# Kernel optimization log

Measured on AMD Instinct MI355X. Metric: run time of the kernel, lower is better.

Reference implementation:

```python
import jax, jax.numpy as jnp
import numpy as np

B, N, M, C = 4, 4096, 300, 1152
SA_H, SA_D = 36, 32           # linear self-attention heads / head dim
CA_H = 16                     # cross-attention heads
INNER_SA = SA_H * SA_D        # 1152
INNER_FF = int(C * 2.5)       # 2880
EPS = 1e-6


def _ln(x):
    # LayerNorm without affine, eps=1e-6
    mu = x.mean(-1, keepdims=True)
    var = x.var(-1, keepdims=True)
    return (x - mu) / jnp.sqrt(var + EPS)


def setup_inputs() -> dict:
    key = jax.random.key(0)
    ks = jax.random.split(key, 24)
    p = lambda i, shape: jax.random.normal(ks[i], shape, jnp.float32) * 0.02
    return {
        "x": jax.random.normal(ks[0], (B, N, C), jnp.float32),
        "conditioning": jax.random.normal(ks[1], (B, M, C), jnp.float32),
        "t_emb": jax.random.normal(ks[2], (B, C), jnp.float32),
        # linear self-attention (qkv has no bias)
        "w_qkv": p(3, (C, 3 * INNER_SA)),
        "w_sa_out": p(4, (INNER_SA, C)),
        "b_sa_out": jnp.zeros((C,), jnp.float32),
        # norm_cross (affine LayerNorm)
        "gamma_cross": jnp.ones((C,), jnp.float32),
        "beta_cross": jnp.zeros((C,), jnp.float32),
        # cross-attention
        "w_q": p(5, (C, C)), "b_q": jnp.zeros((C,), jnp.float32),
        "w_kv": p(6, (C, 2 * C)), "b_kv": jnp.zeros((2 * C,), jnp.float32),
        "w_co": p(7, (C, C)), "b_co": jnp.zeros((C,), jnp.float32),
        # MixFFN
        "w_fc1": p(8, (C, 2 * INNER_FF)), "b_fc1": jnp.zeros((2 * INNER_FF,), jnp.float32),
        "dw_kernel": p(9, (3, 3, 1, INNER_FF)),  # depthwise conv, HWIO
        "dw_bias": jnp.zeros((INNER_FF,), jnp.float32),
        "w_fc2": p(10, (INNER_FF, C)), "b_fc2": jnp.zeros((C,), jnp.float32),
        # adaLN modulation
        "w_ada": p(11, (C, 6 * C)), "b_ada": jnp.zeros((6 * C,), jnp.float32),
        "sst": jax.random.normal(ks[12], (6, C), jnp.float32) * 0.02,
    }


def reference(x, conditioning, t_emb, w_qkv, w_sa_out, b_sa_out,
              gamma_cross, beta_cross, w_q, b_q, w_kv, b_kv, w_co, b_co,
              w_fc1, b_fc1, dw_kernel, dw_bias, w_fc2, b_fc2,
              w_ada, b_ada, sst):
    Bx, Nx, Cx = x.shape
    ada = jax.nn.silu(t_emb) @ w_ada + b_ada          # (B, 6C)
    ada = sst[None] + ada.reshape(Bx, 6, Cx)          # (B, 6, C)
    shift_sa, scale_sa, gate_sa, shift_ff, scale_ff, gate_ff = (
        ada[:, 0], ada[:, 1], ada[:, 2], ada[:, 3], ada[:, 4], ada[:, 5])

    # --- modulated linear self-attention (ReLU kernel) ---
    xn = _ln(x) * (1.0 + scale_sa[:, None]) + shift_sa[:, None]
    qkv = (xn @ w_qkv).reshape(Bx, Nx, 3, SA_H, SA_D)
    q = jax.nn.relu(qkv[:, :, 0])
    k = jax.nn.relu(qkv[:, :, 1])
    v = qkv[:, :, 2]
    kv = jnp.einsum('bnhd,bnhe->bhde', k, v)                  # (B,H,D,D)
    out = jnp.einsum('bnhd,bhde->bnhe', q, kv)                # (B,N,H,D)
    denom = jnp.einsum('bnhd,bhd->bnh', q, k.sum(1)) + 1e-6   # (B,N,H)
    out = (out / denom[..., None]).reshape(Bx, Nx, INNER_SA)
    x = x + gate_sa[:, None] * (out @ w_sa_out + b_sa_out)

    # --- cross-attention (softmax) ---
    xc = _ln(x) * gamma_cross + beta_cross
    hd = Cx // CA_H
    qc = (xc @ w_q + b_q).reshape(Bx, Nx, CA_H, hd)
    kvc = (conditioning @ w_kv + b_kv).reshape(Bx, M, 2, CA_H, hd)
    kc, vc = kvc[:, :, 0], kvc[:, :, 1]
    attn = jnp.einsum('bnhd,bmhd->bhnm', qc, kc) * (hd ** -0.5)
    attn = jax.nn.softmax(attn, axis=-1)
    oc = jnp.einsum('bhnm,bmhd->bnhd', attn, vc).reshape(Bx, Nx, Cx)
    x = x + oc @ w_co + b_co

    # --- modulated GLU-dwconv FFN ---
    xn = _ln(x) * (1.0 + scale_ff[:, None]) + shift_ff[:, None]
    gv = xn @ w_fc1 + b_fc1
    gate, val = gv[..., :INNER_FF], gv[..., INNER_FF:]
    h = jax.nn.silu(gate) * val
    hw = int(round(Nx ** 0.5))
    h = h.reshape(Bx, hw, hw, INNER_FF)                       # NHWC
    h = jax.lax.conv_general_dilated(
        h, dw_kernel, window_strides=(1, 1), padding='SAME',
        dimension_numbers=('NHWC', 'HWIO', 'NHWC'),
        feature_group_count=INNER_FF) + dw_bias
    h = h.reshape(Bx, Nx, INNER_FF)
    x = x + gate_ff[:, None] * (h @ w_fc2 + b_fc2)
    return x
```

## Files before the change

kernel.cpp:

```cpp
#include <hip/hip_runtime.h>

typedef __bf16 bf16_t;
typedef __attribute__((ext_vector_type(8))) __bf16 bf16x8;
typedef __attribute__((ext_vector_type(4))) __bf16 bf16x4;
typedef __attribute__((ext_vector_type(4))) float f32x4;

#define DEVINL __device__ __forceinline__

DEVINL void gload16(const void* g, void* l) {
  __builtin_amdgcn_global_load_lds(
      (const __attribute__((address_space(1))) void*)g,
      (__attribute__((address_space(3))) void*)l, 16, 0, 0);
}

template <int OUT>
__global__ __launch_bounds__(512) void gemm256(
    const bf16_t* __restrict__ A, const bf16_t* __restrict__ Bt,
    void* __restrict__ Cv, int M, int N, int K,
    const float* __restrict__ bias, const float* __restrict__ resid,
    const float* __restrict__ gate, int GM)
{
  __shared__ __align__(16) bf16_t sA[2][256 * 64];
  __shared__ __align__(16) bf16_t sB[2][256 * 64];
  const int tid = threadIdx.x;
  const int lane = tid & 63;
  const int wave = tid >> 6;
  const int wr = wave >> 2;
  const int wc = wave & 3;

  const int nbx = gridDim.x, nby = gridDim.y;
  const int nwg = nbx * nby;
  int lin = (int)blockIdx.y * nbx + (int)blockIdx.x;
  {
    const int q = nwg >> 3, r = nwg & 7;
    const int xcd = lin & 7, idx = lin >> 3;
    lin = (xcd < r ? xcd * (q + 1) : r * (q + 1) + (xcd - r) * q) + idx;
  }
  const int per_grp = GM * nbx;
  const int gid = lin / per_grp;
  const int rem = lin - gid * per_grp;
  const int gsz = min(GM, nby - gid * GM);
  const long tileM = (long)(gid * GM + rem % gsz) * 256;
  const long tileN = (long)(rem / gsz) * 256;

  int arow[4], acol[4];
#pragma unroll
  for (int j = 0; j < 4; ++j) {
    const int ch = tid + j * 512;
    const int r = ch >> 3;
    arow[j] = r;
    acol[j] = ((ch & 7) ^ (r & 7)) * 8;
  }

  auto STAGE = [&](int buf, int kt) {
#pragma unroll
    for (int j = 0; j < 4; ++j)
      gload16(A + (tileM + arow[j]) * (long)K + kt + acol[j],
              (char*)(&sA[buf][0]) + (tid + j * 512) * 16);
#pragma unroll
    for (int j = 0; j < 4; ++j)
      gload16(Bt + (tileN + arow[j]) * (long)K + kt + acol[j],
              (char*)(&sB[buf][0]) + (tid + j * 512) * 16);
  };

  f32x4 acc[8][4] = {};
  const int NT = K >> 6;

  STAGE(0, 0);
  STAGE(1, 64);
  asm volatile("s_waitcnt vmcnt(8)" ::: "memory");
  asm volatile("s_barrier" ::: "memory");

  const int lrow = lane & 15;
  const int lkbase = (lane >> 4) << 4;
  const int lxor = (lane & 7) << 4;

  for (int t = 0; t < NT; ++t) {
    const char* pA = (const char*)(&sA[t & 1][0]);
    const char* pB = (const char*)(&sB[t & 1][0]);
#pragma unroll
    for (int ks = 0; ks < 2; ++ks) {
      const int koff = ((ks << 6) | lkbase) ^ lxor;
      bf16x8 a[8], b[4];
#pragma unroll
      for (int n = 0; n < 4; ++n)
        b[n] = *(const bf16x8*)(pB + (wc * 64 + n * 16 + lrow) * 128 + koff);
#pragma unroll
      for (int m = 0; m < 8; ++m)
        a[m] = *(const bf16x8*)(pA + (wr * 128 + m * 16 + lrow) * 128 + koff);
      __builtin_amdgcn_s_setprio(1);
#pragma unroll
      for (int m = 0; m < 8; ++m)
#pragma unroll
        for (int n = 0; n < 4; ++n)
          acc[m][n] = __builtin_amdgcn_mfma_f32_16x16x32_bf16(a[m], b[n],
                                                              acc[m][n], 0, 0, 0);
      __builtin_amdgcn_s_setprio(0);
    }
    __builtin_amdgcn_sched_barrier(0);
    asm volatile("s_barrier" ::: "memory");
    if (t + 2 < NT) {
      STAGE(t & 1, (t + 2) << 6);
      asm volatile("s_waitcnt vmcnt(8)" ::: "memory");
    } else {
      asm volatile("s_waitcnt vmcnt(0)" ::: "memory");
    }
    asm volatile("s_barrier" ::: "memory");
  }

  const long row0 = tileM + wr * 128 + ((lane >> 4) * 4);
  const int col0 = (int)tileN + wc * 64 + lrow;
#pragma unroll
  for (int m = 0; m < 8; ++m) {
#pragma unroll
    for (int n = 0; n < 4; ++n) {
      const int col = col0 + n * 16;
      if (col < N) {
        const float bb = bias ? bias[col] : 0.0f;
#pragma unroll
        for (int j = 0; j < 4; ++j) {
          const long row = row0 + m * 16 + j;
          const long idx = row * (long)N + col;
          const float v = acc[m][n][j] + bb;
          if constexpr (OUT == 1) {
            const float g = gate ? gate[(row >> 12) * 6912 + col] : 1.0f;
            const float r = resid ? resid[idx] : 0.0f;
            ((float*)Cv)[idx] = r + g * v;
          } else {
            ((bf16_t*)Cv)[idx] = (bf16_t)v;
          }
        }
      }
    }
  }
}

template <int OUT>
__global__ __launch_bounds__(256) void gemm_bt(
    const bf16_t* __restrict__ A, const bf16_t* __restrict__ Bt,
    void* __restrict__ Cv, int M, int N, int K,
    long strideA, long strideB, long strideC,
    const float* __restrict__ bias, int GM)
{
  __shared__ __align__(16) bf16_t sA[128 * 32];
  __shared__ __align__(16) bf16_t sB[128 * 32];
  const int tid = threadIdx.x;
  const int lane = tid & 63;
  const int wave = tid >> 6;
  const bf16_t* Ab = A + (size_t)blockIdx.z * strideA;
  const bf16_t* Bb = Bt + (size_t)blockIdx.z * strideB;

  const int nbx = gridDim.x, nby = gridDim.y;
  const int nwg = nbx * nby;
  int lin = (int)blockIdx.y * nbx + (int)blockIdx.x;
  {
    const int q = nwg >> 3, r = nwg & 7;
    const int xcd = lin & 7, idx = lin >> 3;
    lin = (xcd < r ? xcd * (q + 1) : r * (q + 1) + (xcd - r) * q) + idx;
  }
  const int per_grp = GM * nbx;
  const int gid = lin / per_grp;
  const int rem = lin - gid * per_grp;
  const int gsz = min(GM, nby - gid * GM);
  const long tileM = (long)(gid * GM + rem % gsz) * 128;
  const long tileN = (long)(rem / gsz) * 128;
  const int wr = wave >> 1, wc = wave & 1;

  f32x4 acc[4][4] = {};

  const int srow = lane >> 2;
  const int skcol = (lane & 3) * 8;
  const bf16_t* gA0 = Ab + (tileM + wave * 16 + srow) * (long)K + skcol;
  const bf16_t* gB0 = Bb + (tileN + wave * 16 + srow) * (long)K + skcol;
  bf16_t* lA0 = sA + wave * 512;
  bf16_t* lB0 = sB + wave * 512;
  const long rs64 = 64L * K;

  const int aoff = (wr * 64 + (lane & 15)) * 32 + (lane >> 4) * 8;
  const int boff = (wc * 64 + (lane & 15)) * 32 + (lane >> 4) * 8;

  for (int kt = 0; kt < K; kt += 32) {
    __syncthreads();
    gload16(gA0 + kt, lA0);
    gload16(gA0 + kt + rs64, lA0 + 2048);
    gload16(gB0 + kt, lB0);
    gload16(gB0 + kt + rs64, lB0 + 2048);
    __syncthreads();
    bf16x8 av[4], bv[4];
#pragma unroll
    for (int m = 0; m < 4; ++m) av[m] = *(const bf16x8*)&sA[aoff + m * 512];
#pragma unroll
    for (int n = 0; n < 4; ++n) bv[n] = *(const bf16x8*)&sB[boff + n * 512];
#pragma unroll
    for (int m = 0; m < 4; ++m)
#pragma unroll
      for (int n = 0; n < 4; ++n)
        acc[m][n] = __builtin_amdgcn_mfma_f32_16x16x32_bf16(av[m], bv[n],
                                                            acc[m][n], 0, 0, 0);
  }

  const long row0 = tileM + wr * 64 + ((lane >> 4) * 4);
  const int col0 = (int)tileN + wc * 64 + (lane & 15);
#pragma unroll
  for (int m = 0; m < 4; ++m) {
#pragma unroll
    for (int n = 0; n < 4; ++n) {
      const int col = col0 + n * 16;
      const float bb = (OUT != 2 && bias) ? bias[col] : 0.0f;
#pragma unroll
      for (int j = 0; j < 4; ++j) {
        const long row = row0 + m * 16 + j;
        const float v = acc[m][n][j] + bb;
        if constexpr (OUT == 2) {
          if (col < 72)
            ((bf16_t*)Cv)[row * 1152 + (long)blockIdx.z * 72 + col] = (bf16_t)v;
        } else {
          const long idx = row * (long)N + col;
          (((bf16_t*)Cv) + (size_t)blockIdx.z * strideC)[idx] = (bf16_t)v;
        }
      }
    }
  }
}

__global__ __launch_bounds__(256) void transpose_cast(
    const float* __restrict__ W, bf16_t* __restrict__ WT, int K, int N)
{
  __shared__ float tile[32][33];
  const int n0 = blockIdx.x * 32, k0 = blockIdx.y * 32;
  const int tx = threadIdx.x & 31, ty = threadIdx.x >> 5;
#pragma unroll
  for (int r = ty; r < 32; r += 8) tile[r][tx] = W[(size_t)(k0 + r) * N + n0 + tx];
  __syncthreads();
#pragma unroll
  for (int r = ty; r < 32; r += 8)
    WT[(size_t)(n0 + r) * K + k0 + tx] = (bf16_t)tile[tx][r];
}

__global__ __launch_bounds__(256) void ada_kernel(
    const float* __restrict__ t_emb, const float* __restrict__ w_ada,
    const float* __restrict__ b_ada, const float* __restrict__ sst,
    float* __restrict__ ada)
{
  __shared__ float st[4][1152];
  const int t = threadIdx.x;
  const int j = blockIdx.x * 256 + t;
  for (int i = t; i < 4 * 1152; i += 256) {
    const int b = i / 1152, cc = i % 1152;
    const float v = t_emb[b * 1152 + cc];
    st[b][cc] = v / (1.0f + __expf(-v));
  }
  __syncthreads();
  const int k0 = blockIdx.y * 144;
  float a0 = 0.f, a1 = 0.f, a2 = 0.f, a3 = 0.f;
  for (int k = k0; k < k0 + 144; ++k) {
    const float w = w_ada[(size_t)k * 6912 + j];
    a0 += st[0][k] * w; a1 += st[1][k] * w;
    a2 += st[2][k] * w; a3 += st[3][k] * w;
  }
  if (blockIdx.y == 0) {
    const float base = b_ada[j] + sst[j];
    a0 += base; a1 += base; a2 += base; a3 += base;
  }
  atomicAdd(&ada[0 * 6912 + j], a0);
  atomicAdd(&ada[1 * 6912 + j], a1);
  atomicAdd(&ada[2 * 6912 + j], a2);
  atomicAdd(&ada[3 * 6912 + j], a3);
}

__global__ __launch_bounds__(256) void ln_mod(
    const float* __restrict__ X, bf16_t* __restrict__ out,
    const float* __restrict__ adaB, int shiftIdx, int scaleIdx,
    const float* __restrict__ gamma, const float* __restrict__ beta)
{
  const int row = blockIdx.x;
  const float4* xr4 = (const float4*)(X + (size_t)row * 1152);
  float s = 0.f, s2 = 0.f;
  for (int i = threadIdx.x; i < 288; i += 256) {
    const float4 v = xr4[i];
    s += v.x + v.y + v.z + v.w;
    s2 += v.x * v.x + v.y * v.y + v.z * v.z + v.w * v.w;
  }
  const int lane = threadIdx.x & 63, wave = threadIdx.x >> 6;
#pragma unroll
  for (int o = 32; o; o >>= 1) { s += __shfl_down(s, o); s2 += __shfl_down(s2, o); }
  __shared__ float rs[4], rq[4];
  if (lane == 0) { rs[wave] = s; rq[wave] = s2; }
  __syncthreads();
  if (threadIdx.x == 0) {
    rs[0] = rs[0] + rs[1] + rs[2] + rs[3];
    rq[0] = rq[0] + rq[1] + rq[2] + rq[3];
  }
  __syncthreads();
  const float mu = rs[0] * (1.0f / 1152.0f);
  const float var = rq[0] * (1.0f / 1152.0f) - mu * mu;
  const float inv = rsqrtf(var + 1e-6f);
  const int b = row >> 12;
  const float4* shiftv = (const float4*)(adaB ? adaB + b * 6912 + shiftIdx * 1152 : beta);
  const float4* scalev = (const float4*)(adaB ? adaB + b * 6912 + scaleIdx * 1152 : gamma);
  const float add1 = adaB ? 1.0f : 0.0f;
  for (int i = threadIdx.x; i < 288; i += 256) {
    const float4 v = xr4[i];
    const float4 sc = scalev[i];
    const float4 sh = shiftv[i];
    bf16x4 o;
    o[0] = (bf16_t)((v.x - mu) * inv * (add1 + sc.x) + sh.x);
    o[1] = (bf16_t)((v.y - mu) * inv * (add1 + sc.y) + sh.y);
    o[2] = (bf16_t)((v.z - mu) * inv * (add1 + sc.z) + sh.z);
    o[3] = (bf16_t)((v.w - mu) * inv * (add1 + sc.w) + sh.w);
    *(bf16x4*)&out[(size_t)row * 1152 + i * 4] = o;
  }
}

__global__ void pad_cond_k(const float* __restrict__ cond, bf16_t* __restrict__ condp)
{
  const int idx = blockIdx.x * 256 + threadIdx.x;
  const int row = idx / 1152;
  condp[idx] = (row < 1200) ? (bf16_t)cond[idx] : (bf16_t)0.0f;
}

__global__ __launch_bounds__(256) void sa_kv_k(
    const bf16_t* __restrict__ qkv, float* __restrict__ kvb, float* __restrict__ ksumb)
{
  const int bh = blockIdx.x, b = bh / 36, h = bh % 36;
  __shared__ bf16_t sk[32][32], sv[32][32];
  const int t = threadIdx.x;
  const int nn = t >> 5, c = t & 31;
  const int srow = (t & 127) >> 2;
  const int sq4 = (t & 3) * 8;
  const int isV = t >> 7;
  float a0 = 0.f, a1 = 0.f, a2 = 0.f, a3 = 0.f, ks = 0.f;
  const size_t rowbase = (size_t)b * 4096 + (size_t)blockIdx.y * 256;
  const size_t colbase = 1152 + (size_t)isV * 1152 + h * 32 + sq4;
  for (int n0 = 0; n0 < 256; n0 += 32) {
    __syncthreads();
    const bf16x8 v8 = *(const bf16x8*)&qkv[(rowbase + n0 + srow) * 3456 + colbase];
    if (isV == 0) {
      bf16x8 r8;
#pragma unroll
      for (int j = 0; j < 8; ++j) r8[j] = (bf16_t)fmaxf((float)v8[j], 0.0f);
      *(bf16x8*)&sk[srow][sq4] = r8;
    } else {
      *(bf16x8*)&sv[srow][sq4] = v8;
    }
    __syncthreads();
#pragma unroll
    for (int q = 0; q < 32; ++q) {
      const float vv = (float)sv[q][c];
      a0 += (float)sk[q][nn] * vv;
      a1 += (float)sk[q][nn + 8] * vv;
      a2 += (float)sk[q][nn + 16] * vv;
      a3 += (float)sk[q][nn + 24] * vv;
    }
    if (t < 32) {
#pragma unroll
      for (int q = 0; q < 32; ++q) ks += (float)sk[q][t];
    }
  }
  float* kvp = kvb + (size_t)bh * 1024;
  atomicAdd(&kvp[(nn + 0) * 32 + c], a0);
  atomicAdd(&kvp[(nn + 8) * 32 + c], a1);
  atomicAdd(&kvp[(nn + 16) * 32 + c], a2);
  atomicAdd(&kvp[(nn + 24) * 32 + c], a3);
  if (t < 32) atomicAdd(&ksumb[bh * 32 + t], ks);
}

__global__ __launch_bounds__(256) void sa_out_k(
    const bf16_t* __restrict__ qkv, const float* __restrict__ kvb,
    const float* __restrict__ ksumb, bf16_t* __restrict__ so)
{
  const int row0 = blockIdx.x * 8;
  const int b = row0 >> 12;
  __shared__ float q[8][1152];
  __shared__ float denom[8][36];
  const int t = threadIdx.x;
  for (int i = t; i < 1152; i += 256) {
    const int r = i / 144, c0 = (i % 144) * 8;
    const bf16x8 v8 = *(const bf16x8*)&qkv[(size_t)(row0 + r) * 3456 + c0];
#pragma unroll
    for (int j = 0; j < 8; ++j) q[r][c0 + j] = fmaxf((float)v8[j], 0.0f);
  }
  __syncthreads();
  for (int i = t; i < 288; i += 256) {
    int r = i / 36, h = i % 36;
    const float* ksp = ksumb + (b * 36 + h) * 32;
    float dsum = 1e-6f;
#pragma unroll
    for (int d = 0; d < 32; ++d) dsum += q[r][h * 32 + d] * ksp[d];
    denom[r][h] = dsum;
  }
  __syncthreads();
  for (int j = t; j < 1152; j += 256) {
    const int h = j >> 5, e = j & 31;
    const float* kvp = kvb + ((size_t)(b * 36 + h)) * 1024 + e;
    float kreg[32];
#pragma unroll
    for (int d = 0; d < 32; ++d) kreg[d] = kvp[d * 32];
#pragma unroll
    for (int r = 0; r < 8; ++r) {
      float a = 0.f;
#pragma unroll
      for (int d = 0; d < 32; ++d) a += q[r][h * 32 + d] * kreg[d];
      so[(size_t)(row0 + r) * 1152 + j] = (bf16_t)(a / denom[r][h]);
    }
  }
}

__global__ void ca_qrepack(const bf16_t* __restrict__ qc, bf16_t* __restrict__ qcp, int b)
{
  const size_t idx = (size_t)blockIdx.x * 256 + threadIdx.x;
  const int d = (int)(idx % 96);
  const size_t r = idx / 96;
  const int n = (int)(r & 4095);
  const int h = (int)(r >> 12);
  float v = 0.f;
  if (d < 72) v = (float)qc[((size_t)(b * 4096 + n)) * 1152 + h * 72 + d] * 0.11785113019775793f;
  qcp[idx] = (bf16_t)v;
}

__global__ void ca_kcrepack(const bf16_t* __restrict__ kvc, bf16_t* __restrict__ kcp, int b)
{
  const size_t idx = (size_t)blockIdx.x * 256 + threadIdx.x;
  const int d = (int)(idx % 96);
  const size_t r = idx / 96;
  const int m = (int)(r % 384);
  const int h = (int)(r / 384);
  bf16_t v = (bf16_t)0.0f;
  if (d < 72 && m < 300) v = kvc[((size_t)(b * 300 + m)) * 2304 + h * 72 + d];
  kcp[idx] = v;
}

__global__ void ca_vtrepack(const bf16_t* __restrict__ kvc, bf16_t* __restrict__ vt, int b)
{
  const size_t idx = (size_t)blockIdx.x * 256 + threadIdx.x;
  const int m = (int)(idx % 384);
  const size_t r = idx / 384;
  const int d = (int)(r & 127);
  const int h = (int)(r >> 7);
  bf16_t v = (bf16_t)0.0f;
  if (d < 72 && m < 300) v = kvc[((size_t)(b * 300 + m)) * 2304 + 1152 + h * 72 + d];
  vt[idx] = v;
}

__global__ __launch_bounds__(256) void softmax_k(bf16_t* __restrict__ s)
{
  const int row = blockIdx.x * 4 + (threadIdx.x >> 6);
  const int lane = threadIdx.x & 63;
  bf16_t* sr = s + (size_t)row * 384;
  float v[5];
  float mx = -1e30f;
#pragma unroll
  for (int i = 0; i < 5; ++i) {
    const int m = lane + 64 * i;
    v[i] = (m < 300) ? (float)sr[m] : -1e30f;
    mx = fmaxf(mx, v[i]);
  }
#pragma unroll
  for (int o = 32; o; o >>= 1) mx = fmaxf(mx, __shfl_xor(mx, o));
  float sum = 0.f;
#pragma unroll
  for (int i = 0; i < 5; ++i) { v[i] = __expf(v[i] - mx); sum += v[i]; }
#pragma unroll
  for (int o = 32; o; o >>= 1) sum += __shfl_xor(sum, o);
  const float inv = 1.0f / sum;
#pragma unroll
  for (int i = 0; i < 5; ++i) {
    const int m = lane + 64 * i;
    if (m < 320) sr[m] = (bf16_t)(v[i] * inv);
  }
}

__global__ void glu_k(const bf16_t* __restrict__ gv, bf16_t* __restrict__ h)
{
  const size_t idx = (size_t)blockIdx.x * 256 + threadIdx.x;
  const size_t row = idx / 360;
  const int c0 = (int)(idx % 360) * 8;
  const bf16x8 g8 = *(const bf16x8*)&gv[row * 5760 + c0];
  const bf16x8 v8 = *(const bf16x8*)&gv[row * 5760 + 2880 + c0];
  bf16x8 o;
#pragma unroll
  for (int j = 0; j < 8; ++j) {
    const float g = (float)g8[j];
    const float sg = g / (1.0f + __expf(-g));
    o[j] = (bf16_t)(sg * (float)v8[j]);
  }
  *(bf16x8*)&h[row * 2880 + c0] = o;
}

__global__ __launch_bounds__(256) void dwconv_k(
    const bf16_t* __restrict__ h, const float* __restrict__ wk,
    const float* __restrict__ wb, bf16_t* __restrict__ hc)
{
  const size_t idx = (size_t)blockIdx.x * 256 + threadIdx.x;
  const int c8 = (int)(idx % 360);
  size_t p = idx / 360;
  const int x = (int)(p & 63);
  const int y = (int)(p >> 6);
  const int c0 = c8 * 8;
  float acc[8];
#pragma unroll
  for (int j = 0; j < 8; ++j) acc[j] = wb[c0 + j];
  for (int ky = -1; ky <= 1; ++ky) {
    const int yy = y + ky;
    if (yy < 0 || yy > 63) continue;
    for (int kx = -1; kx <= 1; ++kx) {
      const int xx = x + kx;
      if (xx < 0 || xx > 63) continue;
      const bf16x8 v = *(const bf16x8*)&h[((size_t)(yy * 64 + xx)) * 2880 + c0];
      const float* w = wk + ((ky + 1) * 3 + (kx + 1)) * 2880 + c0;
#pragma unroll
      for (int j = 0; j < 8; ++j) acc[j] += (float)v[j] * w[j];
    }
  }
  bf16x8 o;
#pragma unroll
  for (int j = 0; j < 8; ++j) o[j] = (bf16_t)acc[j];
  *(bf16x8*)&hc[((size_t)(y * 64 + x)) * 2880 + c0] = o;
}

extern "C" void kernel_launch(void* const* d_in, const int* in_sizes, int n_in,
                              void* d_out, int out_size, void* d_ws, size_t ws_size,
                              hipStream_t stream)
{
  const float* x          = (const float*)d_in[0];
  const float* cond       = (const float*)d_in[1];
  const float* t_emb      = (const float*)d_in[2];
  const float* w_qkv      = (const float*)d_in[3];
  const float* w_sa_out   = (const float*)d_in[4];
  const float* b_sa_out   = (const float*)d_in[5];
  const float* gamma_cr   = (const float*)d_in[6];
  const float* beta_cr    = (const float*)d_in[7];
  const float* w_q        = (const float*)d_in[8];
  const float* b_q        = (const float*)d_in[9];
  const float* w_kv       = (const float*)d_in[10];
  const float* b_kv       = (const float*)d_in[11];
  const float* w_co       = (const float*)d_in[12];
  const float* b_co       = (const float*)d_in[13];
  const float* w_fc1      = (const float*)d_in[14];
  const float* b_fc1      = (const float*)d_in[15];
  const float* dw_kernel  = (const float*)d_in[16];
  const float* dw_bias    = (const float*)d_in[17];
  const float* w_fc2      = (const float*)d_in[18];
  const float* b_fc2      = (const float*)d_in[19];
  const float* w_ada      = (const float*)d_in[20];
  const float* b_ada      = (const float*)d_in[21];
  const float* sst        = (const float*)d_in[22];
  float* out = (float*)d_out;

  char* ws = (char*)d_ws;
  size_t off = 0;
  auto alloc = [&](size_t bytes) -> char* {
    off = (off + 255) & ~(size_t)255;
    char* p = ws + off;
    off += bytes;
    return p;
  };

  bf16_t* wqkvT  = (bf16_t*)alloc((size_t)3584 * 1152 * 2);
  bf16_t* wsaT   = (bf16_t*)alloc((size_t)1280 * 1152 * 2);
  bf16_t* wqT    = (bf16_t*)alloc((size_t)1280 * 1152 * 2);
  bf16_t* wkvT   = (bf16_t*)alloc((size_t)2304 * 1152 * 2);
  bf16_t* wcoT   = (bf16_t*)alloc((size_t)1280 * 1152 * 2);
  bf16_t* wfc1T  = (bf16_t*)alloc((size_t)5888 * 1152 * 2);
  bf16_t* wfc2T  = (bf16_t*)alloc((size_t)1280 * 2880 * 2);
  float*  adaB   = (float*)alloc((size_t)4 * 6912 * 4);
  bf16_t* xn     = (bf16_t*)alloc((size_t)16384 * 1152 * 2);
  bf16_t* buf37  = (bf16_t*)alloc((size_t)16384 * 1152 * 2);
  float*  kvb    = (float*)alloc((size_t)144 * 1024 * 4);
  float*  ksumb  = (float*)alloc((size_t)144 * 32 * 4);
  bf16_t* condp  = (bf16_t*)alloc((size_t)1280 * 1152 * 2);
  bf16_t* kvcB   = (bf16_t*)alloc((size_t)1280 * 2304 * 2);
  char* arena = alloc((size_t)16384 * 3456 * 2);

  if (off > ws_size) return;

  bf16_t* qkvB = (bf16_t*)arena;
  bf16_t* qcp    = (bf16_t*)arena;
  bf16_t* kcp    = (bf16_t*)(arena + 12582912);
  bf16_t* vcT    = (bf16_t*)(arena + 12582912 + 1179648);
  bf16_t* scores = (bf16_t*)(arena + 12582912 + 1179648 + 1572864);
  bf16_t* hc2b = (bf16_t*)arena;
  bf16_t* gvB  = (bf16_t*)(arena + (size_t)8192 * 2880 * 2);
  bf16_t* hB   = buf37;

  hipMemsetAsync(adaB, 0, (size_t)4 * 6912 * 4, stream);
  hipMemsetAsync(kvb, 0, (size_t)144 * 1024 * 4, stream);
  hipMemsetAsync(ksumb, 0, (size_t)144 * 32 * 4, stream);

  transpose_cast<<<dim3(108, 36), 256, 0, stream>>>(w_qkv, wqkvT, 1152, 3456);
  transpose_cast<<<dim3(36, 36), 256, 0, stream>>>(w_sa_out, wsaT, 1152, 1152);
  transpose_cast<<<dim3(36, 36), 256, 0, stream>>>(w_q, wqT, 1152, 1152);
  transpose_cast<<<dim3(72, 36), 256, 0, stream>>>(w_kv, wkvT, 1152, 2304);
  transpose_cast<<<dim3(36, 36), 256, 0, stream>>>(w_co, wcoT, 1152, 1152);
  transpose_cast<<<dim3(180, 36), 256, 0, stream>>>(w_fc1, wfc1T, 1152, 5760);
  transpose_cast<<<dim3(36, 90), 256, 0, stream>>>(w_fc2, wfc2T, 2880, 1152);
  ada_kernel<<<dim3(27, 8), 256, 0, stream>>>(t_emb, w_ada, b_ada, sst, adaB);
  pad_cond_k<<<5760, 256, 0, stream>>>(cond, condp);

  ln_mod<<<16384, 256, 0, stream>>>(x, xn, adaB, 0, 1, nullptr, nullptr);
  gemm256<0><<<dim3(14, 64), 512, 0, stream>>>(xn, wqkvT, qkvB, 16384, 3456, 1152,
                                               nullptr, nullptr, nullptr, 8);
  sa_kv_k<<<dim3(144, 16), 256, 0, stream>>>(qkvB, kvb, ksumb);
  sa_out_k<<<2048, 256, 0, stream>>>(qkvB, kvb, ksumb, buf37);
  gemm256<1><<<dim3(5, 64), 512, 0, stream>>>(buf37, wsaT, out, 16384, 1152, 1152,
                                              b_sa_out, x, adaB + 2 * 1152, 8);

  ln_mod<<<16384, 256, 0, stream>>>(out, xn, nullptr, 0, 0, gamma_cr, beta_cr);
  gemm256<0><<<dim3(5, 64), 512, 0, stream>>>(xn, wqT, buf37, 16384, 1152, 1152,
                                              b_q, nullptr, nullptr, 8);
  gemm_bt<0><<<dim3(18, 10, 1), 256, 0, stream>>>(condp, wkvT, kvcB, 1280, 2304, 1152,
                                                  0, 0, 0, b_kv, 8);
  for (int b = 0; b < 4; ++b) {
    ca_qrepack<<<24576, 256, 0, stream>>>(buf37, qcp, b);
    ca_kcrepack<<<2304, 256, 0, stream>>>(kvcB, kcp, b);
    ca_vtrepack<<<3072, 256, 0, stream>>>(kvcB, vcT, b);
    gemm_bt<0><<<dim3(3, 32, 16), 256, 0, stream>>>(qcp, kcp, scores, 4096, 384, 96,
                                                    (long)4096 * 96, (long)384 * 96,
                                                    (long)4096 * 384, nullptr, 8);
    softmax_k<<<16384, 256, 0, stream>>>(scores);
    gemm_bt<2><<<dim3(1, 32, 16), 256, 0, stream>>>(scores, vcT,
                                                    buf37 + (size_t)b * 4096 * 1152,
                                                    4096, 128, 384,
                                                    (long)4096 * 384, (long)128 * 384,
                                                    0, nullptr, 8);
  }
  gemm256<1><<<dim3(5, 64), 512, 0, stream>>>(buf37, wcoT, out, 16384, 1152, 1152,
                                              b_co, out, nullptr, 8);

  ln_mod<<<16384, 256, 0, stream>>>(out, xn, adaB, 3, 4, nullptr, nullptr);
  for (int c = 0; c < 2; ++c) {
    for (int bb = 0; bb < 2; ++bb) {
      const int b = c * 2 + bb;
      gemm256<0><<<dim3(23, 16), 512, 0, stream>>>(xn + (size_t)b * 4096 * 1152, wfc1T,
                                                   gvB, 4096, 5760, 1152,
                                                   b_fc1, nullptr, nullptr, 8);
      glu_k<<<5760, 256, 0, stream>>>(gvB, hB);
      dwconv_k<<<5760, 256, 0, stream>>>(hB, dw_kernel, dw_bias,
                                         hc2b + (size_t)bb * 4096 * 2880);
    }
    gemm256<1><<<dim3(5, 32), 512, 0, stream>>>(hc2b, wfc2T, out + (size_t)c * 8192 * 1152,
                                                8192, 1152, 2880, b_fc2,
                                                out + (size_t)c * 8192 * 1152,
                                                adaB + (size_t)c * 2 * 6912 + 5 * 1152, 8);
  }

  (void)in_sizes; (void)n_in; (void)out_size; (void)ws_size;
}
```

Baseline: 2.065 ms.

## Triple-buffer GEMM with K=32 stages and batch cross-attention and FFN launches

The main GEMM moves from a double-buffered K=64 tile to a triple-buffered K=32 tile with a new LDS swizzle and one barrier per iteration, aiming to hide global-load latency better. When the workspace is large enough, the per-batch cross-attention loop becomes single launches over all 64 batch-heads. The FFN fc1 GEMM also runs over two batches at once. This cuts launch count and gives larger grids, at the cost of a bigger workspace and a fallback path when the workspace is small.

```diff
diff --git a/kernel.cpp b/kernel.cpp
--- a/kernel.cpp
+++ b/kernel.cpp
@@ -14,14 +14,13 @@
 }
 
 template <int OUT>
-__global__ __launch_bounds__(512) void gemm256(
+__global__ __launch_bounds__(512) void gemm256r(
     const bf16_t* __restrict__ A, const bf16_t* __restrict__ Bt,
     void* __restrict__ Cv, int M, int N, int K,
     const float* __restrict__ bias, const float* __restrict__ resid,
     const float* __restrict__ gate, int GM)
 {
-  __shared__ __align__(16) bf16_t sA[2][256 * 64];
-  __shared__ __align__(16) bf16_t sB[2][256 * 64];
+  __shared__ __align__(16) bf16_t sL[3][2][256 * 32];
   const int tid = threadIdx.x;
   const int lane = tid & 63;
   const int wave = tid >> 6;
@@ -32,9 +31,9 @@
   const int nwg = nbx * nby;
   int lin = (int)blockIdx.y * nbx + (int)blockIdx.x;
   {
-    const int q = nwg >> 3, r = nwg & 7;
+    const int q = nwg >> 3, rr = nwg & 7;
     const int xcd = lin & 7, idx = lin >> 3;
-    lin = (xcd < r ? xcd * (q + 1) : r * (q + 1) + (xcd - r) * q) + idx;
+    lin = (xcd < rr ? xcd * (q + 1) : rr * (q + 1) + (xcd - rr) * q) + idx;
   }
   const int per_grp = GM * nbx;
   const int gid = lin / per_grp;
@@ -43,73 +42,60 @@
   const long tileM = (long)(gid * GM + rem % gsz) * 256;
   const long tileN = (long)(rem / gsz) * 256;
 
-  int arow[4], acol[4];
-#pragma unroll
-  for (int j = 0; j < 4; ++j) {
-    const int ch = tid + j * 512;
-    const int r = ch >> 3;
-    arow[j] = r;
-    acol[j] = ((ch & 7) ^ (r & 7)) * 8;
-  }
-
-  auto STAGE = [&](int buf, int kt) {
-#pragma unroll
-    for (int j = 0; j < 4; ++j)
-      gload16(A + (tileM + arow[j]) * (long)K + kt + acol[j],
-              (char*)(&sA[buf][0]) + (tid + j * 512) * 16);
-#pragma unroll
-    for (int j = 0; j < 4; ++j)
-      gload16(Bt + (tileN + arow[j]) * (long)K + kt + acol[j],
-              (char*)(&sB[buf][0]) + (tid + j * 512) * 16);
+  const int r0 = tid >> 2;
+  const int c0 = (((tid & 3) - (r0 >> 2)) & 3) * 8;
+
+  auto STAGE = [&](int slot, int kt) {
+    const bf16_t* ga = A + (tileM + r0) * (long)K + kt + c0;
+    const bf16_t* gb = Bt + (tileN + r0) * (long)K + kt + c0;
+    char* la = (char*)&sL[slot][0][0] + tid * 16;
+    char* lb = (char*)&sL[slot][1][0] + tid * 16;
+    gload16(ga, la);
+    gload16(ga + 128 * (long)K, la + 8192);
+    gload16(gb, lb);
+    gload16(gb + 128 * (long)K, lb + 8192);
   };
 
   f32x4 acc[8][4] = {};
-  const int NT = K >> 6;
-
-  STAGE(0, 0);
-  STAGE(1, 64);
+  const int NT = K >> 5;
+
+  STAGE(0, 0); STAGE(1, 32); STAGE(2, 64);
   asm volatile("s_waitcnt vmcnt(8)" ::: "memory");
   asm volatile("s_barrier" ::: "memory");
 
-  const int lrow = lane & 15;
-  const int lkbase = (lane >> 4) << 4;
-  const int lxor = (lane & 7) << 4;
-
+  const int r = lane & 15;
+  const int kg = lane >> 4;
+  const int sw = ((kg + (r >> 2)) & 3) * 16;
+  const int abyte = (wr * 128 + r) * 64 + sw;
+  const int bbyte = (wc * 64 + r) * 64 + sw;
+
+  int slot = 0;
   for (int t = 0; t < NT; ++t) {
-    const char* pA = (const char*)(&sA[t & 1][0]);
-    const char* pB = (const char*)(&sB[t & 1][0]);
-#pragma unroll
-    for (int ks = 0; ks < 2; ++ks) {
-      const int koff = ((ks << 6) | lkbase) ^ lxor;
-      bf16x8 a[8], b[4];
+    const char* pA = (const char*)&sL[slot][0][0];
+    const char* pB = (const char*)&sL[slot][1][0];
+    bf16x8 a[8], b[4];
+#pragma unroll
+    for (int n = 0; n < 4; ++n) b[n] = *(const bf16x8*)(pB + bbyte + n * 1024);
+#pragma unroll
+    for (int m = 0; m < 8; ++m) a[m] = *(const bf16x8*)(pA + abyte + m * 1024);
+    __builtin_amdgcn_s_setprio(1);
+#pragma unroll
+    for (int m = 0; m < 8; ++m)
 #pragma unroll
       for (int n = 0; n < 4; ++n)
-        b[n] = *(const bf16x8*)(pB + (wc * 64 + n * 16 + lrow) * 128 + koff);
-#pragma unroll
-      for (int m = 0; m < 8; ++m)
-        a[m] = *(const bf16x8*)(pA + (wr * 128 + m * 16 + lrow) * 128 + koff);
-      __builtin_amdgcn_s_setprio(1);
-#pragma unroll
-      for (int m = 0; m < 8; ++m)
-#pragma unroll
-        for (int n = 0; n < 4; ++n)
-          acc[m][n] = __builtin_amdgcn_mfma_f32_16x16x32_bf16(a[m], b[n],
-                                                              acc[m][n], 0, 0, 0);
-      __builtin_amdgcn_s_setprio(0);
-    }
-    __builtin_amdgcn_sched_barrier(0);
+        acc[m][n] = __builtin_amdgcn_mfma_f32_16x16x32_bf16(a[m], b[n],
+                                                            acc[m][n], 0, 0, 0);
+    __builtin_amdgcn_s_setprio(0);
+    if (t + 1 >= NT) break;
+    if (t + 2 < NT) asm volatile("s_waitcnt vmcnt(4)" ::: "memory");
+    else            asm volatile("s_waitcnt vmcnt(0)" ::: "memory");
     asm volatile("s_barrier" ::: "memory");
-    if (t + 2 < NT) {
-      STAGE(t & 1, (t + 2) << 6);
-      asm volatile("s_waitcnt vmcnt(8)" ::: "memory");
-    } else {
-      asm volatile("s_waitcnt vmcnt(0)" ::: "memory");
-    }
-    asm volatile("s_barrier" ::: "memory");
+    if (t + 3 < NT) STAGE(slot, (t + 3) << 5);
+    slot = (slot == 2) ? 0 : slot + 1;
   }
 
   const long row0 = tileM + wr * 128 + ((lane >> 4) * 4);
-  const int col0 = (int)tileN + wc * 64 + lrow;
+  const int col0 = (int)tileN + wc * 64 + r;
 #pragma unroll
   for (int m = 0; m < 8; ++m) {
 #pragma unroll
@@ -124,8 +110,8 @@
           const float v = acc[m][n][j] + bb;
           if constexpr (OUT == 1) {
             const float g = gate ? gate[(row >> 12) * 6912 + col] : 1.0f;
-            const float r = resid ? resid[idx] : 0.0f;
-            ((float*)Cv)[idx] = r + g * v;
+            const float rv = resid ? resid[idx] : 0.0f;
+            ((float*)Cv)[idx] = rv + g * v;
           } else {
             ((bf16_t*)Cv)[idx] = (bf16_t)v;
           }
@@ -154,9 +140,9 @@
   const int nwg = nbx * nby;
   int lin = (int)blockIdx.y * nbx + (int)blockIdx.x;
   {
-    const int q = nwg >> 3, r = nwg & 7;
+    const int q = nwg >> 3, rr = nwg & 7;
     const int xcd = lin & 7, idx = lin >> 3;
-    lin = (xcd < r ? xcd * (q + 1) : r * (q + 1) + (xcd - r) * q) + idx;
+    lin = (xcd < rr ? xcd * (q + 1) : rr * (q + 1) + (xcd - rr) * q) + idx;
   }
   const int per_grp = GM * nbx;
   const int gid = lin / per_grp;
@@ -213,7 +199,8 @@
         const float v = acc[m][n][j] + bb;
         if constexpr (OUT == 2) {
           if (col < 72)
-            ((bf16_t*)Cv)[row * 1152 + (long)blockIdx.z * 72 + col] = (bf16_t)v;
+            ((bf16_t*)Cv)[(((long)(blockIdx.z >> 4)) * 4096 + row) * 1152 +
+                          (long)(blockIdx.z & 15) * 72 + col] = (bf16_t)v;
         } else {
           const long idx = row * (long)N + col;
           (((bf16_t*)Cv) + (size_t)blockIdx.z * strideC)[idx] = (bf16_t)v;
@@ -570,18 +557,40 @@
   float*  ksumb  = (float*)alloc((size_t)144 * 32 * 4);
   bf16_t* condp  = (bf16_t*)alloc((size_t)1280 * 1152 * 2);
   bf16_t* kvcB   = (bf16_t*)alloc((size_t)1280 * 2304 * 2);
-  char* arena = alloc((size_t)16384 * 3456 * 2);
-
+
+  const size_t ARENA_SMALL = (size_t)16384 * 3456 * 2;
+  const size_t CA_Q = (size_t)64 * 4096 * 96 * 2;
+  const size_t CA_K = (size_t)64 * 384 * 96 * 2;
+  const size_t CA_V = (size_t)64 * 128 * 384 * 2;
+  const size_t CA_S = (size_t)64 * 4096 * 384 * 2;
+  const size_t ARENA_BIG = CA_Q + CA_K + CA_V + CA_S;
+  const bool big = (off + 512 + ARENA_BIG) <= ws_size;
+  char* arena = alloc(big ? ARENA_BIG : ARENA_SMALL);
   if (off > ws_size) return;
 
   bf16_t* qkvB = (bf16_t*)arena;
-  bf16_t* qcp    = (bf16_t*)arena;
-  bf16_t* kcp    = (bf16_t*)(arena + 12582912);
-  bf16_t* vcT    = (bf16_t*)(arena + 12582912 + 1179648);
-  bf16_t* scores = (bf16_t*)(arena + 12582912 + 1179648 + 1572864);
-  bf16_t* hc2b = (bf16_t*)arena;
-  bf16_t* gvB  = (bf16_t*)(arena + (size_t)8192 * 2880 * 2);
-  bf16_t* hB   = buf37;
+  bf16_t *qcp, *kcp, *vcT, *scores;
+  if (big) {
+    qcp    = (bf16_t*)arena;
+    kcp    = (bf16_t*)(arena + CA_Q);
+    vcT    = (bf16_t*)(arena + CA_Q + CA_K);
+    scores = (bf16_t*)(arena + CA_Q + CA_K + CA_V);
+  } else {
+    qcp    = (bf16_t*)arena;
+    kcp    = (bf16_t*)(arena + 12582912);
+    vcT    = (bf16_t*)(arena + 12582912 + 1179648);
+    scores = (bf16_t*)(arena + 12582912 + 1179648 + 1572864);
+  }
+  bf16_t *gvB, *hB, *hcB;
+  if (big) {
+    gvB = (bf16_t*)arena;
+    hB  = (bf16_t*)(arena + (size_t)8192 * 5760 * 2);
+    hcB = (bf16_t*)(arena + (size_t)8192 * 5760 * 2 + (size_t)8192 * 2880 * 2);
+  } else {
+    hcB = (bf16_t*)arena;
+    gvB = (bf16_t*)(arena + (size_t)8192 * 2880 * 2);
+    hB  = buf37;
+  }
 
   hipMemsetAsync(adaB, 0, (size_t)4 * 6912 * 4, stream);
   hipMemsetAsync(kvb, 0, (size_t)144 * 1024 * 4, stream);
@@ -598,50 +607,84 @@
   pad_cond_k<<<5760, 256, 0, stream>>>(cond, condp);
 
   ln_mod<<<16384, 256, 0, stream>>>(x, xn, adaB, 0, 1, nullptr, nullptr);
-  gemm256<0><<<dim3(14, 64), 512, 0, stream>>>(xn, wqkvT, qkvB, 16384, 3456, 1152,
-                                               nullptr, nullptr, nullptr, 8);
+  gemm256r<0><<<dim3(14, 64), 512, 0, stream>>>(xn, wqkvT, qkvB, 16384, 3456, 1152,
+                                                nullptr, nullptr, nullptr, 8);
   sa_kv_k<<<dim3(144, 16), 256, 0, stream>>>(qkvB, kvb, ksumb);
   sa_out_k<<<2048, 256, 0, stream>>>(qkvB, kvb, ksumb, buf37);
-  gemm256<1><<<dim3(5, 64), 512, 0, stream>>>(buf37, wsaT, out, 16384, 1152, 1152,
-                                              b_sa_out, x, adaB + 2 * 1152, 8);
+  gemm256r<1><<<dim3(5, 64), 512, 0, stream>>>(buf37, wsaT, out, 16384, 1152, 1152,
+                                               b_sa_out, x, adaB + 2 * 1152, 8);
 
   ln_mod<<<16384, 256, 0, stream>>>(out, xn, nullptr, 0, 0, gamma_cr, beta_cr);
-  gemm256<0><<<dim3(5, 64), 512, 0, stream>>>(xn, wqT, buf37, 16384, 1152, 1152,
-                                              b_q, nullptr, nullptr, 8);
+  gemm256r<0><<<dim3(5, 64), 512, 0, stream>>>(xn, wqT, buf37, 16384, 1152, 1152,
+                                               b_q, nullptr, nullptr, 8);
   gemm_bt<0><<<dim3(18, 10, 1), 256, 0, stream>>>(condp, wkvT, kvcB, 1280, 2304, 1152,
                                                   0, 0, 0, b_kv, 8);
-  for (int b = 0; b < 4; ++b) {
-    ca_qrepack<<<24576, 256, 0, stream>>>(buf37, qcp, b);
-    ca_kcrepack<<<2304, 256, 0, stream>>>(kvcB, kcp, b);
-    ca_vtrepack<<<3072, 256, 0, stream>>>(kvcB, vcT, b);
-    gemm_bt<0><<<dim3(3, 32, 16), 256, 0, stream>>>(qcp, kcp, scores, 4096, 384, 96,
+  if (big) {
+    for (int b = 0; b < 4; ++b) {
+      ca_qrepack<<<24576, 256, 0, stream>>>(buf37, qcp + (size_t)b * 16 * 4096 * 96, b);
+      ca_kcrepack<<<2304, 256, 0, stream>>>(kvcB, kcp + (size_t)b * 16 * 384 * 96, b);
+      ca_vtrepack<<<3072, 256, 0, stream>>>(kvcB, vcT + (size_t)b * 16 * 128 * 384, b);
+    }
+    gemm_bt<0><<<dim3(3, 32, 64), 256, 0, stream>>>(qcp, kcp, scores, 4096, 384, 96,
                                                     (long)4096 * 96, (long)384 * 96,
                                                     (long)4096 * 384, nullptr, 8);
-    softmax_k<<<16384, 256, 0, stream>>>(scores);
-    gemm_bt<2><<<dim3(1, 32, 16), 256, 0, stream>>>(scores, vcT,
-                                                    buf37 + (size_t)b * 4096 * 1152,
-                                                    4096, 128, 384,
+    softmax_k<<<65536, 256, 0, stream>>>(scores);
+    gemm_bt<2><<<dim3(1, 32, 64), 256, 0, stream>>>(scores, vcT, buf37, 4096, 128, 384,
                                                     (long)4096 * 384, (long)128 * 384,
                                                     0, nullptr, 8);
-  }
-  gemm256<1><<<dim3(5, 64), 512, 0, stream>>>(buf37, wcoT, out, 16384, 1152, 1152,
-                                              b_co, out, nullptr, 8);
+  } else {
+    for (int b = 0; b < 4; ++b) {
+      ca_qrepack<<<24576, 256, 0, stream>>>(buf37, qcp, b);
+      ca_kcrepack<<<2304, 256, 0, stream>>>(kvcB, kcp, b);
+      ca_vtrepack<<<3072, 256, 0, stream>>>(kvcB, vcT, b);
+      gemm_bt<0><<<dim3(3, 32, 16), 256, 0, stream>>>(qcp, kcp, scores, 4096, 384, 96,
+                                                      (long)4096 * 96, (long)384 * 96,
+                                                      (long)4096 * 384, nullptr, 8);
+      softmax_k<<<16384, 256, 0, stream>>>(scores);
+      gemm_bt<2><<<dim3(1, 32, 16), 256, 0, stream>>>(scores, vcT,
+                                                      buf37 + (size_t)b * 4096 * 1152,
+                                                      4096, 128, 384,
+                                                      (long)4096 * 384, (long)128 * 384,
+                                                      0, nullptr, 8);
+    }
+  }
+  gemm256r<1><<<dim3(5, 64), 512, 0, stream>>>(buf37, wcoT, out, 16384, 1152, 1152,
+                                               b_co, out, nullptr, 8);
 
   ln_mod<<<16384, 256, 0, stream>>>(out, xn, adaB, 3, 4, nullptr, nullptr);
-  for (int c = 0; c < 2; ++c) {
-    for (int bb = 0; bb < 2; ++bb) {
-      const int b = c * 2 + bb;
-      gemm256<0><<<dim3(23, 16), 512, 0, stream>>>(xn + (size_t)b * 4096 * 1152, wfc1T,
-                                                   gvB, 4096, 5760, 1152,
-                                                   b_fc1, nullptr, nullptr, 8);
-      glu_k<<<5760, 256, 0, stream>>>(gvB, hB);
-      dwconv_k<<<5760, 256, 0, stream>>>(hB, dw_kernel, dw_bias,
-                                         hc2b + (size_t)bb * 4096 * 2880);
-    }
-    gemm256<1><<<dim3(5, 32), 512, 0, stream>>>(hc2b, wfc2T, out + (size_t)c * 8192 * 1152,
-                                                8192, 1152, 2880, b_fc2,
-                                                out + (size_t)c * 8192 * 1152,
-                                                adaB + (size_t)c * 2 * 6912 + 5 * 1152, 8);
+  if (big) {
+    for (int c = 0; c < 2; ++c) {
+      gemm256r<0><<<dim3(23, 32), 512, 0, stream>>>(xn + (size_t)c * 8192 * 1152, wfc1T,
+                                                    gvB, 8192, 5760, 1152,
+                                                    b_fc1, nullptr, nullptr, 8);
+      glu_k<<<11520, 256, 0, stream>>>(gvB, hB);
+      for (int bb = 0; bb < 2; ++bb)
+        dwconv_k<<<5760, 256, 0, stream>>>(hB + (size_t)bb * 4096 * 2880,
+                                           dw_kernel, dw_bias,
+                                           hcB + (size_t)bb * 4096 * 2880);
+      gemm256r<1><<<dim3(5, 32), 512, 0, stream>>>(hcB, wfc2T,
+                                                   out + (size_t)c * 8192 * 1152,
+                                                   8192, 1152, 2880, b_fc2,
+                                                   out + (size_t)c * 8192 * 1152,
+                                                   adaB + (size_t)c * 2 * 6912 + 5 * 1152, 8);
+    }
+  } else {
+    for (int c = 0; c < 2; ++c) {
+      for (int bb = 0; bb < 2; ++bb) {
+        const int b = c * 2 + bb;
+        gemm256r<0><<<dim3(23, 16), 512, 0, stream>>>(xn + (size_t)b * 4096 * 1152, wfc1T,
+                                                      gvB, 4096, 5760, 1152,
+                                                      b_fc1, nullptr, nullptr, 8);
+        glu_k<<<5760, 256, 0, stream>>>(gvB, hB);
+        dwconv_k<<<5760, 256, 0, stream>>>(hB, dw_kernel, dw_bias,
+                                           hcB + (size_t)bb * 4096 * 2880);
+      }
+      gemm256r<1><<<dim3(5, 32), 512, 0, stream>>>(hcB, wfc2T,
+                                                   out + (size_t)c * 8192 * 1152,
+                                                   8192, 1152, 2880, b_fc2,
+                                                   out + (size_t)c * 8192 * 1152,
+                                                   adaB + (size_t)c * 2 * 6912 + 5 * 1152, 8);
+    }
   }
 
   (void)in_sizes; (void)n_in; (void)out_size; (void)ws_size;
```

Result: faster. 1.968 ms (-4.7%).
